# Kernel optimization log

Hardware: AMD Instinct MI355X
Metric: run time of the kernel (lower is better)

The kernel has to match this reference:

```python
import jax, jax.numpy as jnp
import numpy as np

N = 50000
E = 800000
IN_C = 128
HID_C = 64
OUT_C = 64
HEADS = 4
NEG_SLOPE = 0.2


def setup_inputs() -> dict:
    key = jax.random.key(0)
    ks = jax.random.split(key, 12)
    x = jax.random.normal(ks[0], (N, IN_C), dtype=jnp.float32)
    edge_index = jax.random.randint(ks[1], (2, E), 0, N, dtype=jnp.int32)
    s = 0.1
    # layer 1 params (GATConv: shared lin for src/dst, att vectors per head, bias over H*C)
    W1 = jax.random.normal(ks[2], (IN_C, HEADS * HID_C), dtype=jnp.float32) * s
    att_src1 = jax.random.normal(ks[3], (HEADS, HID_C), dtype=jnp.float32) * s
    att_dst1 = jax.random.normal(ks[4], (HEADS, HID_C), dtype=jnp.float32) * s
    b1 = jnp.zeros((HEADS * HID_C,), dtype=jnp.float32)
    # layer 2 params
    W2 = jax.random.normal(ks[5], (HEADS * HID_C, HEADS * OUT_C), dtype=jnp.float32) * s
    att_src2 = jax.random.normal(ks[6], (HEADS, OUT_C), dtype=jnp.float32) * s
    att_dst2 = jax.random.normal(ks[7], (HEADS, OUT_C), dtype=jnp.float32) * s
    b2 = jnp.zeros((HEADS * OUT_C,), dtype=jnp.float32)
    return {"x": x, "edge_index": edge_index,
            "W1": W1, "att_src1": att_src1, "att_dst1": att_dst1, "b1": b1,
            "W2": W2, "att_src2": att_src2, "att_dst2": att_dst2, "b2": b2}


def _segment_softmax(e, dst, n):
    # e: [E, H], softmax over edges sharing the same dst node, per head
    m = jax.ops.segment_max(e, dst, num_segments=n)        # [N, H]
    ex = jnp.exp(e - m[dst])
    z = jax.ops.segment_sum(ex, dst, num_segments=n)       # [N, H]
    return ex / (z[dst] + 1e-16)


def _gat_layer(x, src, dst, W, att_src, att_dst, bias, heads, out_c):
    n = x.shape[0]
    h = (x @ W).reshape(n, heads, out_c)                   # [N, H, C]
    a_s = jnp.einsum('nhc,hc->nh', h, att_src)             # [N, H]
    a_d = jnp.einsum('nhc,hc->nh', h, att_dst)
    e = jax.nn.leaky_relu(a_s[src] + a_d[dst], NEG_SLOPE)  # [E, H]
    alpha = _segment_softmax(e, dst, n)                    # [E, H]
    msg = alpha[:, :, None] * h[src]                       # [E, H, C]
    out = jax.ops.segment_sum(msg, dst, num_segments=n)    # [N, H, C]
    return out.reshape(n, heads * out_c) + bias


def reference(x, edge_index, W1, att_src1, att_dst1, b1, W2, att_src2, att_dst2, b2):
    # PyG GATConv adds self-loops by default
    loops = jnp.arange(N, dtype=edge_index.dtype)
    src = jnp.concatenate([edge_index[0], loops])
    dst = jnp.concatenate([edge_index[1], loops])
    h = jax.nn.elu(_gat_layer(x, src, dst, W1, att_src1, att_dst1, b1, HEADS, HID_C))
    out = jax.nn.elu(_gat_layer(h, src, dst, W2, att_src2, att_dst2, b2, HEADS, OUT_C))
    return out  # [N, HEADS*OUT_C]
```

## Files before the change

kernel.cpp:

```cpp
#include <hip/hip_runtime.h>
#include <hip/hip_fp16.h>
#include <math.h>


#define LEAKY_SLOPE 0.2f

typedef __attribute__((ext_vector_type(8))) short short8v;
typedef __attribute__((ext_vector_type(4))) float float4v;


__global__ void hist_kernel(const int* __restrict__ ei, int* __restrict__ cnt,
                            int E, int Etot) {
    int e = blockIdx.x * blockDim.x + threadIdx.x;
    if (e >= Etot) return;
    int dst = (e < E) ? ei[E + e] : (e - E);
    atomicAdd(&cnt[dst], 1);
}

__global__ __launch_bounds__(1024) void scan_block(const int* __restrict__ cnt,
                                                   int* __restrict__ row_start,
                                                   int* __restrict__ partials,
                                                   int n) {
    __shared__ int wsum[16];
    int tid = threadIdx.x, lane = tid & 63, wid = tid >> 6;
    int gi = blockIdx.x * 1024 + tid;
    int v = (gi < n) ? cnt[gi] : 0;
    int x = v;
#pragma unroll
    for (int off = 1; off < 64; off <<= 1) {
        int y = __shfl_up(x, off, 64);
        if (lane >= off) x += y;
    }
    if (lane == 63) wsum[wid] = x;
    __syncthreads();
    if (wid == 0 && lane < 16) {
        int w = wsum[lane];
#pragma unroll
        for (int off = 1; off < 16; off <<= 1) {
            int y = __shfl_up(w, off, 16);
            if (lane >= off) w += y;
        }
        wsum[lane] = w;
    }
    __syncthreads();
    int excl = x - v + ((wid > 0) ? wsum[wid - 1] : 0);
    if (gi < n) row_start[gi] = excl;
    if (tid == 1023) partials[blockIdx.x] = wsum[15];
}

__global__ void scan_partials(int* __restrict__ partials, int nb) {
    int lane = threadIdx.x;
    int v = (lane < nb) ? partials[lane] : 0;
    int x = v;
#pragma unroll
    for (int off = 1; off < 64; off <<= 1) {
        int y = __shfl_up(x, off, 64);
        if (lane >= off) x += y;
    }
    if (lane < nb) partials[lane] = x - v;
    if (lane == nb - 1) partials[nb] = x;
}

__global__ __launch_bounds__(1024) void scan_add(int* __restrict__ row_start,
                                                 const int* __restrict__ partials,
                                                 int n, int nb) {
    int gi = blockIdx.x * 1024 + threadIdx.x;
    if (gi < n) row_start[gi] += partials[blockIdx.x];
    if (gi == 0) row_start[n] = partials[nb];
}

__global__ void scatter_kernel(const int* __restrict__ ei,
                               const int* __restrict__ row_start,
                               int* __restrict__ fill,
                               int2* __restrict__ edge_sd, int E, int Etot) {
    int e = blockIdx.x * blockDim.x + threadIdx.x;
    if (e >= Etot) return;
    int src, dst;
    if (e < E) { src = ei[e]; dst = ei[E + e]; }
    else       { src = e - E; dst = e - E; }
    int pos = row_start[dst] + atomicAdd(&fill[dst], 1);
    edge_sd[pos] = make_int2(src, dst);
}

__global__ void fill_rec(const int2* __restrict__ edge_sd,
                         const __half* __restrict__ a_s_h,
                         const float* __restrict__ a_d,
                         uint4* __restrict__ rec, int Etot) {
    int i = blockIdx.x * blockDim.x + threadIdx.x;
    if (i >= Etot) return;
    int2 sd = edge_sd[i];
    uint2 as2 = *(const uint2*)&a_s_h[(size_t)sd.x * 4];
    float4 ad4 = *(const float4*)&a_d[(size_t)sd.y * 4];
    float2 f01 = __half22float2(*(const __half2*)&as2.x);
    float2 f23 = __half22float2(*(const __half2*)&as2.y);
    float e0 = f01.x + ad4.x, e1 = f01.y + ad4.y;
    float e2 = f23.x + ad4.z, e3 = f23.y + ad4.w;
    e0 = (e0 > 0.f) ? e0 : LEAKY_SLOPE * e0;
    e1 = (e1 > 0.f) ? e1 : LEAKY_SLOPE * e1;
    e2 = (e2 > 0.f) ? e2 : LEAKY_SLOPE * e2;
    e3 = (e3 > 0.f) ? e3 : LEAKY_SLOPE * e3;
    __half2 w01 = __floats2half2_rn(__expf(e0), __expf(e1));
    __half2 w23 = __floats2half2_rn(__expf(e2), __expf(e3));
    uint4 r = {(unsigned)sd.x, *(unsigned*)&w01, *(unsigned*)&w23, 0u};
    rec[i] = r;
}


__device__ __forceinline__ short bf16_rne(float f) {
    unsigned u = __float_as_uint(f);
    return (short)((u + 0x7FFFu + ((u >> 16) & 1u)) >> 16);
}

__device__ __forceinline__ void split_bf16(float f, short& hi, short& lo) {
    unsigned u = __float_as_uint(f);
    hi = (short)(u >> 16);
    float fhi = __uint_as_float(u & 0xFFFF0000u);
    float flo = f - fhi;
    lo = (short)(__float_as_uint(flo) >> 16);
}

__global__ void split_B(const float* __restrict__ B, short* __restrict__ Bt_hi,
                        short* __restrict__ Bt_lo, int K) {
    int idx = blockIdx.x * 256 + threadIdx.x;
    if (idx >= K * 256) return;
    int k = idx >> 8, c = idx & 255;
    short hi, lo;
    split_bf16(B[idx], hi, lo);
    Bt_hi[c * K + k] = hi;
    Bt_lo[c * K + k] = lo;
}


template <int K, bool ABF16>
__global__ __launch_bounds__(256) void gemm_mfma(
    const void* __restrict__ Ap, const short* __restrict__ Bt_hi,
    const short* __restrict__ Bt_lo, __half* __restrict__ Ch,
    const float* __restrict__ att_src, const float* __restrict__ att_dst,
    __half* __restrict__ a_s_out, float* __restrict__ a_d_out, int M) {
    __shared__ short As_hi[128][40];
    __shared__ short Bs_hi[128][40];
    __shared__ short Bs_lo[128][40];

    const int col0 = (blockIdx.x & 1) * 128;
    const int row0 = (blockIdx.x >> 1) * 128;
    const int tid = threadIdx.x;
    const int lane = tid & 63;
    const int wave = tid >> 6;
    const int wr = wave >> 1, wc = wave & 1;
    const int quad = lane >> 4, lc = lane & 15;

    float4v acc[4][4] = {};

    for (int k0 = 0; k0 < K; k0 += 32) {
        if constexpr (ABF16) {
            const short* Abf = (const short*)Ap;
#pragma unroll
            for (int i = 0; i < 2; i++) {
                int slot = tid + i * 256;
                int r = slot >> 2;
                int ko = (slot & 3) * 8;
                short8v v = {};
                int gr = row0 + r;
                if (gr < M) v = *(const short8v*)&Abf[(size_t)gr * K + k0 + ko];
                *(short8v*)&As_hi[r][ko] = v;
            }
        } else {
            const float* A = (const float*)Ap;
#pragma unroll
            for (int i = 0; i < 4; i++) {
                int slot = tid + i * 256;
                int r = slot >> 3;
                int kq = (slot & 7) * 4;
                float4 v = {0.f, 0.f, 0.f, 0.f};
                int gr = row0 + r;
                if (gr < M) v = *(const float4*)&A[(size_t)gr * K + k0 + kq];
                short4 h4;
                h4.x = bf16_rne(v.x); h4.y = bf16_rne(v.y);
                h4.z = bf16_rne(v.z); h4.w = bf16_rne(v.w);
                *(short4*)&As_hi[r][kq] = h4;
            }
        }
#pragma unroll
        for (int i = 0; i < 2; i++) {
            int slot = tid + i * 256;
            int r = slot >> 2;
            int ko = (slot & 3) * 8;
            size_t gb = (size_t)(col0 + r) * K + k0 + ko;
            short8v vh = *(const short8v*)&Bt_hi[gb];
            short8v vl = *(const short8v*)&Bt_lo[gb];
            *(short8v*)&Bs_hi[r][ko] = vh;
            *(short8v*)&Bs_lo[r][ko] = vl;
        }
        __syncthreads();

        short8v a_hi[4], b_hi[4], b_lo[4];
#pragma unroll
        for (int mt = 0; mt < 4; mt++) {
            int r = wr * 64 + mt * 16 + lc;
            a_hi[mt] = *(const short8v*)&As_hi[r][quad * 8];
        }
#pragma unroll
        for (int nt = 0; nt < 4; nt++) {
            int n = wc * 64 + nt * 16 + lc;
            b_hi[nt] = *(const short8v*)&Bs_hi[n][quad * 8];
            b_lo[nt] = *(const short8v*)&Bs_lo[n][quad * 8];
        }
#pragma unroll
        for (int mt = 0; mt < 4; mt++)
#pragma unroll
            for (int nt = 0; nt < 4; nt++) {
                acc[mt][nt] = __builtin_amdgcn_mfma_f32_16x16x32_bf16(
                    a_hi[mt], b_hi[nt], acc[mt][nt], 0, 0, 0);
                acc[mt][nt] = __builtin_amdgcn_mfma_f32_16x16x32_bf16(
                    a_hi[mt], b_lo[nt], acc[mt][nt], 0, 0, 0);
            }
        __syncthreads();
    }

    const int head = (col0 >> 6) + wc;
    float as_c[4], ad_c[4];
#pragma unroll
    for (int nt = 0; nt < 4; nt++) {
        as_c[nt] = att_src[head * 64 + nt * 16 + lc];
        ad_c[nt] = att_dst[head * 64 + nt * 16 + lc];
    }

#pragma unroll
    for (int mt = 0; mt < 4; mt++) {
#pragma unroll
        for (int r = 0; r < 4; r++) {
            int gr = row0 + wr * 64 + mt * 16 + quad * 4 + r;
            float ps = 0.f, pd = 0.f;
#pragma unroll
            for (int nt = 0; nt < 4; nt++) {
                float c = acc[mt][nt][r];
                ps = fmaf(c, as_c[nt], ps);
                pd = fmaf(c, ad_c[nt], pd);
                if (gr < M)
                    Ch[(size_t)gr * 256 + col0 + wc * 64 + nt * 16 + lc] =
                        __float2half(c);
            }
#pragma unroll
            for (int off = 1; off < 16; off <<= 1) {
                ps += __shfl_xor(ps, off, 64);
                pd += __shfl_xor(pd, off, 64);
            }
            if (lc == 0 && gr < M) {
                a_s_out[gr * 4 + head] = __float2half(ps);
                a_d_out[gr * 4 + head] = pd;
            }
        }
    }
}


template <bool OUT_BF16>
__global__ __launch_bounds__(256) void gat_aggregate(
    const __half* __restrict__ hh, const uint4* __restrict__ rec,
    const int* __restrict__ row_start, const float* __restrict__ bias,
    void* __restrict__ outp, int n) {
    int node = (blockIdx.x * blockDim.x + threadIdx.x) >> 6;
    if (node >= n) return;
    int lane = threadIdx.x & 63;
    int head = lane >> 4;

    int beg = row_start[node];
    int end = row_start[node + 1];
    int em1 = end - 1;

    float l = 0.f;
    float acc[4] = {};

    uint4 r0 = rec[beg];
    uint4 r1 = rec[min(beg + 1, em1)];
    uint4 r2 = rec[min(beg + 2, em1)];
    uint4 r3 = rec[min(beg + 3, em1)];

#define GATH(rr) (*(const uint2*)&hh[(size_t)(rr).x * 256 + lane * 4])
#define PROC(rr, vv)                                                      \
    {                                                                     \
        unsigned u = (head & 2) ? (rr).z : (rr).y;                        \
        unsigned short us = (head & 1) ? (unsigned short)(u >> 16)        \
                                       : (unsigned short)(u & 0xFFFFu);   \
        float w = __half2float(*(const __half*)&us);                      \
        l += w;                                                           \
        const __half2* hp = (const __half2*)&(vv);                        \
        float2 f0 = __half22float2(hp[0]);                                \
        float2 f1 = __half22float2(hp[1]);                                \
        acc[0] = fmaf(w, f0.x, acc[0]);                                   \
        acc[1] = fmaf(w, f0.y, acc[1]);                                   \
        acc[2] = fmaf(w, f1.x, acc[2]);                                   \
        acc[3] = fmaf(w, f1.y, acc[3]);                                   \
    }

    uint2 h0 = GATH(r0);
    uint2 h1 = GATH(r1);
    uint2 h2 = GATH(r2);
    uint2 h3;

    int s = beg;
    while (s < end) {
        h3 = GATH(r3);
        PROC(r0, h0);
        r0 = rec[min(s + 4, em1)];
        if (++s >= end) break;
        h0 = GATH(r0);
        PROC(r1, h1);
        r1 = rec[min(s + 4, em1)];
        if (++s >= end) break;
        h1 = GATH(r1);
        PROC(r2, h2);
        r2 = rec[min(s + 4, em1)];
        if (++s >= end) break;
        h2 = GATH(r2);
        PROC(r3, h3);
        r3 = rec[min(s + 4, em1)];
        ++s;
    }
#undef GATH
#undef PROC

    float rcp = 1.f / l;
    float4 b = *(const float4*)&bias[lane * 4];
    float o[4];
    o[0] = fmaf(acc[0], rcp, b.x);
    o[1] = fmaf(acc[1], rcp, b.y);
    o[2] = fmaf(acc[2], rcp, b.z);
    o[3] = fmaf(acc[3], rcp, b.w);
#pragma unroll
    for (int j = 0; j < 4; j++)
        o[j] = (o[j] > 0.f) ? o[j] : __expf(o[j]) - 1.f;
    if constexpr (OUT_BF16) {
        short ob[4];
#pragma unroll
        for (int j = 0; j < 4; j++) ob[j] = bf16_rne(o[j]);
        short* outb = (short*)outp;
        *(short4*)&outb[(size_t)node * 256 + lane * 4] = *(short4*)&ob[0];
    } else {
        float* outf = (float*)outp;
        *(float4*)&outf[(size_t)node * 256 + lane * 4] = *(float4*)&o[0];
    }
}


extern "C" void kernel_launch(void* const* d_in, const int* in_sizes, int n_in,
                              void* d_out, int out_size, void* d_ws, size_t ws_size,
                              hipStream_t stream) {
    const float* x   = (const float*)d_in[0];
    const int*   ei  = (const int*)d_in[1];
    const float* W1  = (const float*)d_in[2];
    const float* as1 = (const float*)d_in[3];
    const float* ad1 = (const float*)d_in[4];
    const float* b1  = (const float*)d_in[5];
    const float* W2  = (const float*)d_in[6];
    const float* as2 = (const float*)d_in[7];
    const float* ad2 = (const float*)d_in[8];
    const float* b2  = (const float*)d_in[9];
    float* out = (float*)d_out;

    const int N = in_sizes[0] / 128;
    const int E = in_sizes[1] / 2;
    const int Etot = E + N;
    const int NB = (N + 1023) / 1024;

    __half* h_half = (__half*)d_ws;
    short*  x1_bf  = (short*)(h_half + (size_t)N * 256);
    uint4*  rec    = (uint4*)(x1_bf + (size_t)N * 256);
    __half* a_s_h  = (__half*)(rec + Etot);
    float*  a_d    = (float*)(a_s_h + (size_t)N * 4);
    short*  Bt1h   = (short*)(a_d + (size_t)N * 4);
    short*  Bt1l   = Bt1h + 256 * 128;
    short*  Bt2h   = Bt1l + 256 * 128;
    short*  Bt2l   = Bt2h + 256 * 256;
    int*    cnt    = (int*)(Bt2l + 256 * 256);
    int*    fill   = cnt + N;
    int*    row_st = fill + N;
    int2*   edge_sd = (int2*)(row_st + (N + 2));
    int*    partials = (int*)(edge_sd + Etot);

    split_B<<<128, 256, 0, stream>>>(W1, Bt1h, Bt1l, 128);
    split_B<<<256, 256, 0, stream>>>(W2, Bt2h, Bt2l, 256);

    hipMemsetAsync(cnt, 0, sizeof(int) * 2 * (size_t)N, stream);
    int eblocks = (Etot + 255) / 256;
    hist_kernel<<<eblocks, 256, 0, stream>>>(ei, cnt, E, Etot);
    scan_block<<<NB, 1024, 0, stream>>>(cnt, row_st, partials, N);
    scan_partials<<<1, 64, 0, stream>>>(partials, NB);
    scan_add<<<NB, 1024, 0, stream>>>(row_st, partials, N, NB);
    scatter_kernel<<<eblocks, 256, 0, stream>>>(ei, row_st, fill, edge_sd, E, Etot);

    dim3 ggrid(2 * ((N + 127) / 128));
    int ablocks = (N + 3) / 4;

    gemm_mfma<128, false><<<ggrid, 256, 0, stream>>>(x, Bt1h, Bt1l, h_half,
                                                     as1, ad1, a_s_h, a_d, N);
    fill_rec<<<eblocks, 256, 0, stream>>>(edge_sd, a_s_h, a_d, rec, Etot);
    gat_aggregate<true><<<ablocks, 256, 0, stream>>>(h_half, rec, row_st,
                                                     b1, x1_bf, N);
    gemm_mfma<256, true><<<ggrid, 256, 0, stream>>>(x1_bf, Bt2h, Bt2l, h_half,
                                                    as2, ad2, a_s_h, a_d, N);
    fill_rec<<<eblocks, 256, 0, stream>>>(edge_sd, a_s_h, a_d, rec, Etot);
    gat_aggregate<false><<<ablocks, 256, 0, stream>>>(h_half, rec, row_st,
                                                      b2, out, N);
}
```

Measured before the change: 420.6 us.

## Split aggregation wave into two half-waves over alternating edges; merge weight-split launches

The aggregate kernel now has each half of the 64-lane wave process alternate edges, with 16-byte gathers of 8 halves per lane, and combines the partial sums with cross-half shuffles before normalisation. This gives more edges in flight per node and wider loads, at the cost of a shuffle reduction and idle lanes in the epilogue. The two weight-split launches are also fused into a single kernel launch to cut launch overhead.

Result: faster. 402.1 us (-4.4%).

```diff
diff --git a/kernel.cpp b/kernel.cpp
--- a/kernel.cpp
+++ b/kernel.cpp
@@ -119,15 +119,24 @@
     lo = (short)(__float_as_uint(flo) >> 16);
 }
 
-__global__ void split_B(const float* __restrict__ B, short* __restrict__ Bt_hi,
-                        short* __restrict__ Bt_lo, int K) {
+__global__ void split_B2(const float* __restrict__ W1, short* __restrict__ Bt1h,
+                         short* __restrict__ Bt1l, const float* __restrict__ W2,
+                         short* __restrict__ Bt2h, short* __restrict__ Bt2l) {
     int idx = blockIdx.x * 256 + threadIdx.x;
-    if (idx >= K * 256) return;
-    int k = idx >> 8, c = idx & 255;
-    short hi, lo;
-    split_bf16(B[idx], hi, lo);
-    Bt_hi[c * K + k] = hi;
-    Bt_lo[c * K + k] = lo;
+    if (idx < 128 * 256) {
+        int k = idx >> 8, c = idx & 255;
+        short hi, lo;
+        split_bf16(W1[idx], hi, lo);
+        Bt1h[c * 128 + k] = hi;
+        Bt1l[c * 128 + k] = lo;
+    } else {
+        int j = idx - 128 * 256;
+        int k = j >> 8, c = j & 255;
+        short hi, lo;
+        split_bf16(W2[j], hi, lo);
+        Bt2h[c * 256 + k] = hi;
+        Bt2l[c * 256 + k] = lo;
+    }
 }
 
 
@@ -262,83 +271,92 @@
     int node = (blockIdx.x * blockDim.x + threadIdx.x) >> 6;
     if (node >= n) return;
     int lane = threadIdx.x & 63;
-    int head = lane >> 4;
+    int half = lane >> 5, l32 = lane & 31;
+    int head = l32 >> 3;
 
     int beg = row_start[node];
     int end = row_start[node + 1];
     int em1 = end - 1;
 
     float l = 0.f;
-    float acc[4] = {};
-
-    uint4 r0 = rec[beg];
-    uint4 r1 = rec[min(beg + 1, em1)];
-    uint4 r2 = rec[min(beg + 2, em1)];
-    uint4 r3 = rec[min(beg + 3, em1)];
-
-#define GATH(rr) (*(const uint2*)&hh[(size_t)(rr).x * 256 + lane * 4])
-#define PROC(rr, vv)                                                      \
+    float acc[8] = {};
+
+    uint4 r0 = rec[min(beg + half, em1)];
+    uint4 r1 = rec[min(beg + 2 + half, em1)];
+    uint4 r2 = rec[min(beg + 4 + half, em1)];
+
+#define GATH(rr) (*(const uint4*)&hh[(size_t)(rr).x * 256 + l32 * 8])
+#define PROC(rr, vv, pp)                                                  \
     {                                                                     \
         unsigned u = (head & 2) ? (rr).z : (rr).y;                        \
         unsigned short us = (head & 1) ? (unsigned short)(u >> 16)        \
                                        : (unsigned short)(u & 0xFFFFu);   \
         float w = __half2float(*(const __half*)&us);                      \
+        w = ((pp) + half < end) ? w : 0.f;                                \
         l += w;                                                           \
         const __half2* hp = (const __half2*)&(vv);                        \
         float2 f0 = __half22float2(hp[0]);                                \
         float2 f1 = __half22float2(hp[1]);                                \
-        acc[0] = fmaf(w, f0.x, acc[0]);                                   \
-        acc[1] = fmaf(w, f0.y, acc[1]);                                   \
-        acc[2] = fmaf(w, f1.x, acc[2]);                                   \
-        acc[3] = fmaf(w, f1.y, acc[3]);                                   \
-    }
-
-    uint2 h0 = GATH(r0);
-    uint2 h1 = GATH(r1);
-    uint2 h2 = GATH(r2);
-    uint2 h3;
-
-    int s = beg;
-    while (s < end) {
-        h3 = GATH(r3);
-        PROC(r0, h0);
-        r0 = rec[min(s + 4, em1)];
-        if (++s >= end) break;
+        float2 f2 = __half22float2(hp[2]);                                \
+        float2 f3 = __half22float2(hp[3]);                                \
+        acc[0] = fmaf(w, f0.x, acc[0]); acc[1] = fmaf(w, f0.y, acc[1]);   \
+        acc[2] = fmaf(w, f1.x, acc[2]); acc[3] = fmaf(w, f1.y, acc[3]);   \
+        acc[4] = fmaf(w, f2.x, acc[4]); acc[5] = fmaf(w, f2.y, acc[5]);   \
+        acc[6] = fmaf(w, f3.x, acc[6]); acc[7] = fmaf(w, f3.y, acc[7]);   \
+    }
+
+    uint4 h0 = GATH(r0);
+    uint4 h1 = GATH(r1);
+    uint4 h2;
+
+    int p = beg;
+    while (p < end) {
+        h2 = GATH(r2);
+        PROC(r0, h0, p);
+        r0 = rec[min(p + 6 + half, em1)];
+        p += 2;
+        if (p >= end) break;
         h0 = GATH(r0);
-        PROC(r1, h1);
-        r1 = rec[min(s + 4, em1)];
-        if (++s >= end) break;
+        PROC(r1, h1, p);
+        r1 = rec[min(p + 6 + half, em1)];
+        p += 2;
+        if (p >= end) break;
         h1 = GATH(r1);
-        PROC(r2, h2);
-        r2 = rec[min(s + 4, em1)];
-        if (++s >= end) break;
-        h2 = GATH(r2);
-        PROC(r3, h3);
-        r3 = rec[min(s + 4, em1)];
-        ++s;
+        PROC(r2, h2, p);
+        r2 = rec[min(p + 6 + half, em1)];
+        p += 2;
     }
 #undef GATH
 #undef PROC
 
-    float rcp = 1.f / l;
-    float4 b = *(const float4*)&bias[lane * 4];
-    float o[4];
-    o[0] = fmaf(acc[0], rcp, b.x);
-    o[1] = fmaf(acc[1], rcp, b.y);
-    o[2] = fmaf(acc[2], rcp, b.z);
-    o[3] = fmaf(acc[3], rcp, b.w);
-#pragma unroll
-    for (int j = 0; j < 4; j++)
-        o[j] = (o[j] > 0.f) ? o[j] : __expf(o[j]) - 1.f;
-    if constexpr (OUT_BF16) {
-        short ob[4];
-#pragma unroll
-        for (int j = 0; j < 4; j++) ob[j] = bf16_rne(o[j]);
-        short* outb = (short*)outp;
-        *(short4*)&outb[(size_t)node * 256 + lane * 4] = *(short4*)&ob[0];
-    } else {
-        float* outf = (float*)outp;
-        *(float4*)&outf[(size_t)node * 256 + lane * 4] = *(float4*)&o[0];
+    l += __shfl_xor(l, 32);
+#pragma unroll
+    for (int j = 0; j < 8; j++) acc[j] += __shfl_xor(acc[j], 32);
+
+    if (half == 0) {
+        float rcp = 1.f / l;
+        float4 b0 = *(const float4*)&bias[l32 * 8];
+        float4 b1 = *(const float4*)&bias[l32 * 8 + 4];
+        float o[8];
+        o[0] = fmaf(acc[0], rcp, b0.x); o[1] = fmaf(acc[1], rcp, b0.y);
+        o[2] = fmaf(acc[2], rcp, b0.z); o[3] = fmaf(acc[3], rcp, b0.w);
+        o[4] = fmaf(acc[4], rcp, b1.x); o[5] = fmaf(acc[5], rcp, b1.y);
+        o[6] = fmaf(acc[6], rcp, b1.z); o[7] = fmaf(acc[7], rcp, b1.w);
+#pragma unroll
+        for (int j = 0; j < 8; j++)
+            o[j] = (o[j] > 0.f) ? o[j] : __expf(o[j]) - 1.f;
+        if constexpr (OUT_BF16) {
+            short ob[8];
+#pragma unroll
+            for (int j = 0; j < 8; j++) ob[j] = bf16_rne(o[j]);
+            short* outb = (short*)outp;
+            *(short4*)&outb[(size_t)node * 256 + l32 * 8] = *(short4*)&ob[0];
+            *(short4*)&outb[(size_t)node * 256 + l32 * 8 + 4] = *(short4*)&ob[4];
+        } else {
+            float* outf = (float*)outp;
+            *(float4*)&outf[(size_t)node * 256 + l32 * 8] = *(float4*)&o[0];
+            *(float4*)&outf[(size_t)node * 256 + l32 * 8 + 4] = *(float4*)&o[4];
+        }
     }
 }
 
@@ -378,8 +396,7 @@
     int2*   edge_sd = (int2*)(row_st + (N + 2));
     int*    partials = (int*)(edge_sd + Etot);
 
-    split_B<<<128, 256, 0, stream>>>(W1, Bt1h, Bt1l, 128);
-    split_B<<<256, 256, 0, stream>>>(W2, Bt2h, Bt2l, 256);
+    split_B2<<<384, 256, 0, stream>>>(W1, Bt1h, Bt1l, W2, Bt2h, Bt2l);
 
     hipMemsetAsync(cnt, 0, sizeof(int) * 2 * (size_t)N, stream);
     int eblocks = (Etot + 255) / 256;
```
